# Kernel optimization log

Hardware: AMD Instinct MI355X
Metric: run time of the kernel (lower is better)

## Reference

```python
import jax, jax.numpy as jnp
import numpy as np

D_MODEL = 1024
NUM_HEADS = 16
HEAD_DIM = D_MODEL // NUM_HEADS
SCALE = 1.0 / np.sqrt(HEAD_DIM).astype(np.float32)


def setup_inputs() -> dict:
    key = jax.random.key(0)
    k1, k2, k3, k4 = jax.random.split(key, 4)
    B, L = 1, 4096
    s = 0.02
    x = jax.random.normal(k1, (B, L, D_MODEL), dtype=jnp.float32)
    W_qkv = jax.random.normal(k2, (D_MODEL, 3 * D_MODEL), dtype=jnp.float32) * s
    W_o = jax.random.normal(k3, (D_MODEL, D_MODEL), dtype=jnp.float32) * s
    b_o = jax.random.normal(k4, (D_MODEL,), dtype=jnp.float32) * s
    return {"x": x, "W_qkv": W_qkv, "W_o": W_o, "b_o": b_o}


def reference(x, W_qkv, W_o, b_o):
    B, L, D = x.shape
    H, Hd = NUM_HEADS, HEAD_DIM
    qkv = x @ W_qkv                          # [B, L, 3D]
    qkv = qkv.reshape(B, L, 3, H, Hd)
    q = jnp.transpose(qkv[:, :, 0], (0, 2, 1, 3))  # [B, H, L, Hd]
    k = jnp.transpose(qkv[:, :, 1], (0, 2, 1, 3))
    v = jnp.transpose(qkv[:, :, 2], (0, 2, 1, 3))
    scores = jnp.einsum("bhqd,bhkd->bhqk", q, k) * SCALE  # [B, H, L, L]
    attn = jax.nn.softmax(scores, axis=-1)
    out = jnp.einsum("bhqk,bhkd->bhqd", attn, v)          # [B, H, L, Hd]
    out = jnp.transpose(out, (0, 2, 1, 3)).reshape(B, L, D)
    return out @ W_o + b_o
```

## Files before the change

### kernel.cpp

```cpp
#include <hip/hip_runtime.h>
#include <stdint.h>


#define L_SEQ 4096
#define DM 1024
#define NHEAD 16
#define HDIM 64
#define ATT_SCALE 0.125f
#define LOG2E 1.4426950408889634f
#define CSC (ATT_SCALE * LOG2E)

typedef __attribute__((ext_vector_type(8))) __bf16 bf16x8;
typedef __attribute__((ext_vector_type(4))) __bf16 bf16x4;
typedef __attribute__((ext_vector_type(4))) float f32x4;
typedef __attribute__((ext_vector_type(8))) float f32x8;
typedef __attribute__((ext_vector_type(4))) short short4v;
typedef __attribute__((ext_vector_type(8))) short short8v;

#define GLL16(g, l) __builtin_amdgcn_global_load_lds( \
    (__attribute__((address_space(1))) void*)(g),     \
    (__attribute__((address_space(3))) void*)(l), 16, 0, 0)

#define MFMA32(a, b, c) __builtin_amdgcn_mfma_f32_16x16x32_bf16((a), (b), (c), 0, 0, 0)

__device__ __forceinline__ short f2bf(float f) {
  uint32_t u = __builtin_bit_cast(uint32_t, f);
  u += 0x7fffu + ((u >> 16) & 1u);
  return (short)(u >> 16);
}

__global__ __launch_bounds__(256)
void prep_kernel(const float* __restrict__ x, short* __restrict__ xb,
                 const float* __restrict__ Wq, short* __restrict__ wqt,
                 const float* __restrict__ Wo, short* __restrict__ wot) {
  __shared__ __align__(16) short tbuf[64 * 66];
  const int tid = threadIdx.x;
  const int blk = blockIdx.x;
  if (blk < 4096) {
    int i = blk * 256 + tid;
    float4 v = ((const float4*)x)[i];
    short4 o;
    o.x = f2bf(v.x); o.y = f2bf(v.y); o.z = f2bf(v.z); o.w = f2bf(v.w);
    ((short4*)xb)[i] = o;
    return;
  }
  const float* W; short* Wt; int N, nb, kb;
  const int K = 1024;
  if (blk < 4096 + 768) {
    int b = blk - 4096;
    W = Wq; Wt = wqt; N = 3072; nb = (b % 48) * 64; kb = (b / 48) * 64;
  } else {
    int b = blk - (4096 + 768);
    W = Wo; Wt = wot; N = 1024; nb = (b % 16) * 64; kb = (b / 16) * 64;
  }
#pragma unroll
  for (int i = 0; i < 16; i++) {
    int idx = tid + i * 256;
    int r = idx >> 6, c = idx & 63;
    tbuf[r * 66 + c] = f2bf(W[(size_t)(kb + r) * N + nb + c]);
  }
  __syncthreads();
#pragma unroll
  for (int i = 0; i < 16; i++) {
    int idx = tid + i * 256;
    int r = idx >> 6, c = idx & 63;
    Wt[(size_t)(nb + r) * K + kb + c] = tbuf[c * 66 + r];
  }
}

__global__ __launch_bounds__(256, 2)
void gemm_qkv(const short* __restrict__ A, const short* __restrict__ Bt,
              short* __restrict__ qkv, short* __restrict__ vtout, int K) {
  __shared__ __align__(16) short As[4096];
  __shared__ __align__(16) short Bs[4096];
  const int tid = threadIdx.x;
  const int lane = tid & 63;
  const int wave = tid >> 6;
  const int quad = lane >> 4;
  const int cl = lane & 15;
  const int m0 = blockIdx.x * 128;
  const int n0 = blockIdx.y * 128;
  const int wm = (wave >> 1) * 64;
  const int wn = (wave & 1) * 64;

  f32x4 acc[4][4] = {};

  for (int kb = 0; kb < K; kb += 32) {
    __syncthreads();
#pragma unroll
    for (int i = 0; i < 2; i++) {
      int ci = i * 256 + tid;
      int row = ci & 127, c = ci >> 7;
      GLL16(A + (size_t)(m0 + row) * K + kb + c * 8, As + ci * 8);
      GLL16(Bt + (size_t)(n0 + row) * K + kb + c * 8, Bs + ci * 8);
    }
    __syncthreads();
    bf16x8 af[4], bfr[4];
#pragma unroll
    for (int t = 0; t < 4; t++) {
      af[t]  = *(const bf16x8*)(As + (quad * 128 + wm + t * 16 + cl) * 8);
      bfr[t] = *(const bf16x8*)(Bs + (quad * 128 + wn + t * 16 + cl) * 8);
    }
#pragma unroll
    for (int mt = 0; mt < 4; mt++)
#pragma unroll
      for (int nt = 0; nt < 4; nt++)
        acc[mt][nt] = MFMA32(af[mt], bfr[nt], acc[mt][nt]);
  }

#pragma unroll
  for (int mt = 0; mt < 4; mt++)
#pragma unroll
    for (int nt = 0; nt < 4; nt++) {
      int col = n0 + wn + nt * 16 + cl;
      int which = col >> 10, hd = col & 63;
      int hidx = (col >> 6) & 15;
      int row0 = m0 + wm + mt * 16 + quad * 4;
      if (which == 2) {
        short4v pk;
#pragma unroll
        for (int r = 0; r < 4; r++) pk[r] = f2bf(acc[mt][nt][r]);
        *(short4v*)(vtout + ((size_t)hidx * HDIM + hd) * L_SEQ + row0) = pk;
      } else {
        float sc = (which == 0) ? CSC : 1.0f;
        size_t base = (((size_t)which * NHEAD + hidx) * L_SEQ) * HDIM + hd;
#pragma unroll
        for (int r = 0; r < 4; r++)
          qkv[base + (size_t)(row0 + r) * HDIM] = f2bf(acc[mt][nt][r] * sc);
      }
    }
}

__global__ __launch_bounds__(256, 2)
void gemm_out(const short* __restrict__ A, const short* __restrict__ Bt,
              float* __restrict__ C, const float* __restrict__ bias, int K) {
  __shared__ __align__(16) short As[4096];
  __shared__ __align__(16) short Bs[2048];
  const int tid = threadIdx.x;
  const int lane = tid & 63;
  const int wave = tid >> 6;
  const int quad = lane >> 4;
  const int cl = lane & 15;
  const int m0 = blockIdx.x * 128;
  const int n0 = blockIdx.y * 64;
  const int wm = (wave >> 1) * 64;
  const int wn = (wave & 1) * 32;
  const int N = 1024;

  f32x4 acc[4][2] = {};

  for (int kb = 0; kb < K; kb += 32) {
    __syncthreads();
#pragma unroll
    for (int i = 0; i < 2; i++) {
      int ci = i * 256 + tid;
      GLL16(A + (size_t)(m0 + (ci & 127)) * K + kb + (ci >> 7) * 8, As + ci * 8);
    }
    GLL16(Bt + (size_t)(n0 + (tid & 63)) * K + kb + (tid >> 6) * 8, Bs + tid * 8);
    __syncthreads();
    bf16x8 af[4], bfr[2];
#pragma unroll
    for (int t = 0; t < 4; t++)
      af[t] = *(const bf16x8*)(As + (quad * 128 + wm + t * 16 + cl) * 8);
#pragma unroll
    for (int t = 0; t < 2; t++)
      bfr[t] = *(const bf16x8*)(Bs + (quad * 64 + wn + t * 16 + cl) * 8);
#pragma unroll
    for (int mt = 0; mt < 4; mt++)
#pragma unroll
      for (int nt = 0; nt < 2; nt++)
        acc[mt][nt] = MFMA32(af[mt], bfr[nt], acc[mt][nt]);
  }

#pragma unroll
  for (int mt = 0; mt < 4; mt++)
#pragma unroll
    for (int nt = 0; nt < 2; nt++) {
      int col = n0 + wn + nt * 16 + cl;
      float b = bias[col];
#pragma unroll
      for (int r = 0; r < 4; r++) {
        int row = m0 + wm + mt * 16 + quad * 4 + r;
        C[(size_t)row * N + col] = acc[mt][nt][r] + b;
      }
    }
}

__global__ __launch_bounds__(256, 4)
void attn_kernel(const short* __restrict__ qkv, const short* __restrict__ vt,
                 short* __restrict__ aout) {
  __shared__ __align__(16) short Ks[2][4096];
  __shared__ __align__(16) short Vs[2][4096];
  const int tid = threadIdx.x, lane = tid & 63, wave = tid >> 6;
  const int quad = lane >> 4, cl = lane & 15;
  const int kg = wave >> 1;
  const int qg = wave & 1;
  const int bid = blockIdx.x;
  const int h  = ((bid & 7) << 1) | ((bid >> 3) & 1);
  const int qb = bid >> 4;
  const short* Qg = qkv + (size_t)h * L_SEQ * HDIM;
  const short* Kg = qkv + ((size_t)NHEAD + h) * L_SEQ * HDIM;
  const short* Vg = vt + (size_t)h * HDIM * L_SEQ;
  const int keyoff = ((cl >> 2) << 3) | (cl & 3);

  bf16x8 qf[2][2];
#pragma unroll
  for (int qs = 0; qs < 2; qs++) {
    int qrow = qb * 64 + qg * 32 + qs * 16 + cl;
    qf[qs][0] = *(const bf16x8*)(Qg + (size_t)qrow * HDIM + quad * 8);
    qf[qs][1] = *(const bf16x8*)(Qg + (size_t)qrow * HDIM + 32 + quad * 8);
  }
  const short8v ov = {0x3F80, 0x3F80, 0x3F80, 0x3F80, 0x3F80, 0x3F80, 0x3F80, 0x3F80};
  const bf16x8 ones = __builtin_bit_cast(bf16x8, ov);
  f32x4 o_l[2] = {};
  f32x4 o_acc[4][2] = {};

  int koff[2][2];
#pragma unroll
  for (int b = 0; b < 2; b++) {
    int krow = kg * 32 + keyoff + b * 4;
    int sw = (krow & 3) | (((krow >> 3) & 1) << 2);
#pragma unroll
    for (int ks = 0; ks < 2; ks++)
      koff[b][ks] = (krow * 8 + ((ks * 4 + quad) ^ sw)) * 8;
  }
  int voff[4];
#pragma unroll
  for (int G = 0; G < 4; G++) {
    int vrow = G * 16 + cl;
    int sw = (vrow & 3) | (((vrow >> 3) & 1) << 2);
    voff[G] = (vrow * 8 + ((kg * 4 + quad) ^ sw)) * 8;
  }

  const short* kp[2]; const short* vp[2]; int ldso[2];
#pragma unroll
  for (int i = 0; i < 2; i++) {
    int ci = i * 256 + tid;
    int row = ci >> 3;
    int sw = (row & 3) | (((row >> 3) & 1) << 2);
    int c = (ci & 7) ^ sw;
    kp[i] = Kg + (size_t)row * HDIM + c * 8;
    vp[i] = Vg + (size_t)row * L_SEQ + c * 8;
    ldso[i] = ci * 8;
  }
#define STAGE(t, buf)                                       \
  {                                                         \
    _Pragma("unroll")                                       \
    for (int i = 0; i < 2; i++) {                           \
      GLL16(kp[i] + (t) * 64 * HDIM, &Ks[buf][ldso[i]]);    \
      GLL16(vp[i] + (t) * 64, &Vs[buf][ldso[i]]);           \
    }                                                       \
  }

  STAGE(0, 0);
#pragma unroll 2
  for (int t = 0; t < L_SEQ / 64; t++) {
    const int cur = t & 1;
    __syncthreads();
    if (t + 1 < L_SEQ / 64) STAGE(t + 1, cur ^ 1);
    const short* Kb = Ks[cur];
    const short* Vb = Vs[cur];

    f32x4 s[2][2] = {};
    __builtin_amdgcn_s_setprio(1);
#pragma unroll
    for (int b = 0; b < 2; b++)
#pragma unroll
      for (int ks = 0; ks < 2; ks++) {
        bf16x8 kf = *(const bf16x8*)(Kb + koff[b][ks]);
#pragma unroll
        for (int qs = 0; qs < 2; qs++)
          s[qs][b] = MFMA32(kf, qf[qs][ks], s[qs][b]);
      }
    __builtin_amdgcn_s_setprio(0);

    bf16x8 vfr[4];
#pragma unroll
    for (int G = 0; G < 4; G++)
      vfr[G] = *(const bf16x8*)(Vb + voff[G]);

    bf16x8 pb0;
    {
      f32x8 pv8;
#pragma unroll
      for (int b = 0; b < 2; b++)
#pragma unroll
        for (int r = 0; r < 4; r++)
          pv8[b * 4 + r] = __builtin_amdgcn_exp2f(s[0][b][r]);
      pb0 = __builtin_convertvector(pv8, bf16x8);
    }

    __builtin_amdgcn_s_setprio(1);
    o_l[0] = MFMA32(ones, pb0, o_l[0]);
#pragma unroll
    for (int G = 0; G < 4; G++)
      o_acc[G][0] = MFMA32(vfr[G], pb0, o_acc[G][0]);
    __builtin_amdgcn_s_setprio(0);

    bf16x8 pb1;
    {
      f32x8 pv8;
#pragma unroll
      for (int b = 0; b < 2; b++)
#pragma unroll
        for (int r = 0; r < 4; r++)
          pv8[b * 4 + r] = __builtin_amdgcn_exp2f(s[1][b][r]);
      pb1 = __builtin_convertvector(pv8, bf16x8);
    }

    __builtin_amdgcn_s_setprio(1);
    o_l[1] = MFMA32(ones, pb1, o_l[1]);
#pragma unroll
    for (int G = 0; G < 4; G++)
      o_acc[G][1] = MFMA32(vfr[G], pb1, o_acc[G][1]);
    __builtin_amdgcn_s_setprio(0);
  }
#undef STAGE

  __syncthreads();
  float* ored = (float*)&Ks[0][0];
  float* lred = (float*)&Vs[0][0];
  if (kg == 1) {
#pragma unroll
    for (int G = 0; G < 4; G++)
#pragma unroll
      for (int qs = 0; qs < 2; qs++)
        *(f32x4*)&ored[(((qg * 4 + G) * 2 + qs) * 64 + lane) * 4] = o_acc[G][qs];
#pragma unroll
    for (int qs = 0; qs < 2; qs++)
      lred[(qg * 2 + qs) * 64 + lane] = o_l[qs][0];
  }
  __syncthreads();
  if (kg == 0) {
#pragma unroll
    for (int qs = 0; qs < 2; qs++) {
      float l = o_l[qs][0] + lred[(qg * 2 + qs) * 64 + lane];
      float inv = 1.f / l;
      int token = qb * 64 + qg * 32 + qs * 16 + cl;
#pragma unroll
      for (int G = 0; G < 4; G++) {
        f32x4 part = *(const f32x4*)&ored[(((qg * 4 + G) * 2 + qs) * 64 + lane) * 4];
        f32x4 sc = (o_acc[G][qs] + part) * inv;
        bf16x4 pk = __builtin_convertvector(sc, bf16x4);
        *(short4v*)(aout + (size_t)token * DM + h * HDIM + G * 16 + quad * 4) =
            __builtin_bit_cast(short4v, pk);
      }
    }
  }
}

extern "C" void kernel_launch(void* const* d_in, const int* in_sizes, int n_in,
                              void* d_out, int out_size, void* d_ws, size_t ws_size,
                              hipStream_t stream) {
  const float* x    = (const float*)d_in[0];
  const float* Wqkv = (const float*)d_in[1];
  const float* Wo   = (const float*)d_in[2];
  const float* bo   = (const float*)d_in[3];
  char* ws = (char*)d_ws;
  short* xb    = (short*)(ws);
  short* wqkvt = (short*)(ws + (size_t)8 * 1024 * 1024);
  short* wot   = (short*)(ws + (size_t)14 * 1024 * 1024);
  short* qkv   = (short*)(ws + (size_t)16 * 1024 * 1024);
  short* vt    = (short*)(ws + (size_t)40 * 1024 * 1024);
  short* aout  = xb;
  float* out = (float*)d_out;

  prep_kernel<<<4096 + 768 + 256, 256, 0, stream>>>(x, xb, Wqkv, wqkvt, Wo, wot);
  gemm_qkv<<<dim3(32, 24), 256, 0, stream>>>(xb, wqkvt, qkv, vt, DM);
  attn_kernel<<<dim3(1024), 256, 0, stream>>>(qkv, vt, aout);
  gemm_out<<<dim3(32, 16), 256, 0, stream>>>(aout, wot, out, bo, DM);
}
```

Baseline: 243.6 us.

## Enlarge attention block to 128 queries and 128-key tiles with 8 waves

The attention kernel now runs 512 threads per block covering 128 query rows, and stages 128-key K/V tiles in shared memory, so each staged tile is reused by twice as many queries. Each wave processes two 32-key slabs per tile, and grid size halves to 512 blocks. The intent is to cut global/L2 K/V traffic and the number of barriers per key. In exchange it doubles LDS per block and halves the block count, which may lower occupancy and leave CUs underfilled.

```diff
diff --git a/kernel.cpp b/kernel.cpp
--- a/kernel.cpp
+++ b/kernel.cpp
@@ -186,15 +186,17 @@
     }
 }
 
-__global__ __launch_bounds__(256, 4)
+#define KVB 128
+__global__ __launch_bounds__(512, 4)
 void attn_kernel(const short* __restrict__ qkv, const short* __restrict__ vt,
                  short* __restrict__ aout) {
-  __shared__ __align__(16) short Ks[2][4096];
-  __shared__ __align__(16) short Vs[2][4096];
+  __shared__ __align__(16) short Ks[2][KVB * HDIM];
+  __shared__ __align__(16) short Vs[2][HDIM * KVB];
+  __shared__ float lbuf[512];
   const int tid = threadIdx.x, lane = tid & 63, wave = tid >> 6;
   const int quad = lane >> 4, cl = lane & 15;
-  const int kg = wave >> 1;
-  const int qg = wave & 1;
+  const int kg = wave & 1;
+  const int qg = wave >> 1;
   const int bid = blockIdx.x;
   const int h  = ((bid & 7) << 1) | ((bid >> 3) & 1);
   const int qb = bid >> 4;
@@ -206,7 +208,7 @@
   bf16x8 qf[2][2];
 #pragma unroll
   for (int qs = 0; qs < 2; qs++) {
-    int qrow = qb * 64 + qg * 32 + qs * 16 + cl;
+    int qrow = qb * 128 + qg * 32 + qs * 16 + cl;
     qf[qs][0] = *(const bf16x8*)(Qg + (size_t)qrow * HDIM + quad * 8);
     qf[qs][1] = *(const bf16x8*)(Qg + (size_t)qrow * HDIM + 32 + quad * 8);
   }
@@ -215,111 +217,121 @@
   f32x4 o_l[2] = {};
   f32x4 o_acc[4][2] = {};
 
-  int koff[2][2];
-#pragma unroll
-  for (int b = 0; b < 2; b++) {
-    int krow = kg * 32 + keyoff + b * 4;
-    int sw = (krow & 3) | (((krow >> 3) & 1) << 2);
-#pragma unroll
-    for (int ks = 0; ks < 2; ks++)
-      koff[b][ks] = (krow * 8 + ((ks * 4 + quad) ^ sw)) * 8;
-  }
-  int voff[4];
-#pragma unroll
-  for (int G = 0; G < 4; G++) {
-    int vrow = G * 16 + cl;
-    int sw = (vrow & 3) | (((vrow >> 3) & 1) << 2);
-    voff[G] = (vrow * 8 + ((kg * 4 + quad) ^ sw)) * 8;
-  }
-
-  const short* kp[2]; const short* vp[2]; int ldso[2];
+  int koff[2][2][2];
+  int voff[2][4];
+#pragma unroll
+  for (int kslab = 0; kslab < 2; kslab++) {
+#pragma unroll
+    for (int b = 0; b < 2; b++) {
+      int krow = kg * 64 + kslab * 32 + keyoff + b * 4;
+      int sw = (krow & 3) | (((krow >> 3) & 1) << 2);
+#pragma unroll
+      for (int ks = 0; ks < 2; ks++)
+        koff[kslab][b][ks] = (krow * 8 + ((ks * 4 + quad) ^ sw)) * 8;
+    }
+#pragma unroll
+    for (int G = 0; G < 4; G++) {
+      int vrow = G * 16 + cl;
+      int sw = (vrow & 3) | (((vrow >> 3) & 1) << 2);
+      voff[kslab][G] = (vrow * 16 + ((kg * 8 + kslab * 4 + quad) ^ sw)) * 8;
+    }
+  }
+
+  const short* kp[2]; const short* vp[2]; int ldsoK[2], ldsoV[2];
 #pragma unroll
   for (int i = 0; i < 2; i++) {
-    int ci = i * 256 + tid;
-    int row = ci >> 3;
-    int sw = (row & 3) | (((row >> 3) & 1) << 2);
-    int c = (ci & 7) ^ sw;
-    kp[i] = Kg + (size_t)row * HDIM + c * 8;
-    vp[i] = Vg + (size_t)row * L_SEQ + c * 8;
-    ldso[i] = ci * 8;
-  }
-#define STAGE(t, buf)                                       \
-  {                                                         \
-    _Pragma("unroll")                                       \
-    for (int i = 0; i < 2; i++) {                           \
-      GLL16(kp[i] + (t) * 64 * HDIM, &Ks[buf][ldso[i]]);    \
-      GLL16(vp[i] + (t) * 64, &Vs[buf][ldso[i]]);           \
-    }                                                       \
+    int ciK = i * 512 + tid;
+    int rowK = ciK >> 3;
+    int swK = (rowK & 3) | (((rowK >> 3) & 1) << 2);
+    int cK = (ciK & 7) ^ swK;
+    kp[i] = Kg + (size_t)rowK * HDIM + cK * 8;
+    ldsoK[i] = ciK * 8;
+    int ciV = i * 512 + tid;
+    int rowV = ciV >> 4;
+    int swV = (rowV & 3) | (((rowV >> 3) & 1) << 2);
+    int cV = (ciV & 15) ^ swV;
+    vp[i] = Vg + (size_t)rowV * L_SEQ + cV * 8;
+    ldsoV[i] = ciV * 8;
+  }
+#define STAGE(t, buf)                                        \
+  {                                                          \
+    _Pragma("unroll")                                        \
+    for (int i = 0; i < 2; i++) {                            \
+      GLL16(kp[i] + (t) * KVB * HDIM, &Ks[buf][ldsoK[i]]);   \
+      GLL16(vp[i] + (t) * KVB, &Vs[buf][ldsoV[i]]);          \
+    }                                                        \
   }
 
   STAGE(0, 0);
 #pragma unroll 2
-  for (int t = 0; t < L_SEQ / 64; t++) {
+  for (int t = 0; t < L_SEQ / KVB; t++) {
     const int cur = t & 1;
     __syncthreads();
-    if (t + 1 < L_SEQ / 64) STAGE(t + 1, cur ^ 1);
+    if (t + 1 < L_SEQ / KVB) STAGE(t + 1, cur ^ 1);
     const short* Kb = Ks[cur];
     const short* Vb = Vs[cur];
 
-    f32x4 s[2][2] = {};
-    __builtin_amdgcn_s_setprio(1);
-#pragma unroll
-    for (int b = 0; b < 2; b++)
-#pragma unroll
-      for (int ks = 0; ks < 2; ks++) {
-        bf16x8 kf = *(const bf16x8*)(Kb + koff[b][ks]);
-#pragma unroll
-        for (int qs = 0; qs < 2; qs++)
-          s[qs][b] = MFMA32(kf, qf[qs][ks], s[qs][b]);
-      }
-    __builtin_amdgcn_s_setprio(0);
-
-    bf16x8 vfr[4];
-#pragma unroll
-    for (int G = 0; G < 4; G++)
-      vfr[G] = *(const bf16x8*)(Vb + voff[G]);
-
-    bf16x8 pb0;
-    {
-      f32x8 pv8;
+#pragma unroll
+    for (int kslab = 0; kslab < 2; kslab++) {
+      f32x4 s[2][2] = {};
+      __builtin_amdgcn_s_setprio(1);
 #pragma unroll
       for (int b = 0; b < 2; b++)
 #pragma unroll
-        for (int r = 0; r < 4; r++)
-          pv8[b * 4 + r] = __builtin_amdgcn_exp2f(s[0][b][r]);
-      pb0 = __builtin_convertvector(pv8, bf16x8);
-    }
-
-    __builtin_amdgcn_s_setprio(1);
-    o_l[0] = MFMA32(ones, pb0, o_l[0]);
-#pragma unroll
-    for (int G = 0; G < 4; G++)
-      o_acc[G][0] = MFMA32(vfr[G], pb0, o_acc[G][0]);
-    __builtin_amdgcn_s_setprio(0);
-
-    bf16x8 pb1;
-    {
-      f32x8 pv8;
-#pragma unroll
-      for (int b = 0; b < 2; b++)
-#pragma unroll
-        for (int r = 0; r < 4; r++)
-          pv8[b * 4 + r] = __builtin_amdgcn_exp2f(s[1][b][r]);
-      pb1 = __builtin_convertvector(pv8, bf16x8);
-    }
-
-    __builtin_amdgcn_s_setprio(1);
-    o_l[1] = MFMA32(ones, pb1, o_l[1]);
-#pragma unroll
-    for (int G = 0; G < 4; G++)
-      o_acc[G][1] = MFMA32(vfr[G], pb1, o_acc[G][1]);
-    __builtin_amdgcn_s_setprio(0);
+        for (int ks = 0; ks < 2; ks++) {
+          bf16x8 kf = *(const bf16x8*)(Kb + koff[kslab][b][ks]);
+#pragma unroll
+          for (int qs = 0; qs < 2; qs++)
+            s[qs][b] = MFMA32(kf, qf[qs][ks], s[qs][b]);
+        }
+      __builtin_amdgcn_s_setprio(0);
+
+      bf16x8 vfr[4];
+#pragma unroll
+      for (int G = 0; G < 4; G++)
+        vfr[G] = *(const bf16x8*)(Vb + voff[kslab][G]);
+
+      bf16x8 pb0;
+      {
+        f32x8 pv8;
+#pragma unroll
+        for (int b = 0; b < 2; b++)
+#pragma unroll
+          for (int r = 0; r < 4; r++)
+            pv8[b * 4 + r] = __builtin_amdgcn_exp2f(s[0][b][r]);
+        pb0 = __builtin_convertvector(pv8, bf16x8);
+      }
+
+      __builtin_amdgcn_s_setprio(1);
+      o_l[0] = MFMA32(ones, pb0, o_l[0]);
+#pragma unroll
+      for (int G = 0; G < 4; G++)
+        o_acc[G][0] = MFMA32(vfr[G], pb0, o_acc[G][0]);
+      __builtin_amdgcn_s_setprio(0);
+
+      bf16x8 pb1;
+      {
+        f32x8 pv8;
+#pragma unroll
+        for (int b = 0; b < 2; b++)
+#pragma unroll
+          for (int r = 0; r < 4; r++)
+            pv8[b * 4 + r] = __builtin_amdgcn_exp2f(s[1][b][r]);
+        pb1 = __builtin_convertvector(pv8, bf16x8);
+      }
+
+      __builtin_amdgcn_s_setprio(1);
+      o_l[1] = MFMA32(ones, pb1, o_l[1]);
+#pragma unroll
+      for (int G = 0; G < 4; G++)
+        o_acc[G][1] = MFMA32(vfr[G], pb1, o_acc[G][1]);
+      __builtin_amdgcn_s_setprio(0);
+    }
   }
 #undef STAGE
 
   __syncthreads();
   float* ored = (float*)&Ks[0][0];
-  float* lred = (float*)&Vs[0][0];
   if (kg == 1) {
 #pragma unroll
     for (int G = 0; G < 4; G++)
@@ -328,15 +340,15 @@
         *(f32x4*)&ored[(((qg * 4 + G) * 2 + qs) * 64 + lane) * 4] = o_acc[G][qs];
 #pragma unroll
     for (int qs = 0; qs < 2; qs++)
-      lred[(qg * 2 + qs) * 64 + lane] = o_l[qs][0];
+      lbuf[(qg * 2 + qs) * 64 + lane] = o_l[qs][0];
   }
   __syncthreads();
   if (kg == 0) {
 #pragma unroll
     for (int qs = 0; qs < 2; qs++) {
-      float l = o_l[qs][0] + lred[(qg * 2 + qs) * 64 + lane];
+      float l = o_l[qs][0] + lbuf[(qg * 2 + qs) * 64 + lane];
       float inv = 1.f / l;
-      int token = qb * 64 + qg * 32 + qs * 16 + cl;
+      int token = qb * 128 + qg * 32 + qs * 16 + cl;
 #pragma unroll
       for (int G = 0; G < 4; G++) {
         f32x4 part = *(const f32x4*)&ored[(((qg * 4 + G) * 2 + qs) * 64 + lane) * 4];
@@ -367,6 +379,6 @@
 
   prep_kernel<<<4096 + 768 + 256, 256, 0, stream>>>(x, xb, Wqkv, wqkvt, Wo, wot);
   gemm_qkv<<<dim3(32, 24), 256, 0, stream>>>(xb, wqkvt, qkv, vt, DM);
-  attn_kernel<<<dim3(1024), 256, 0, stream>>>(qkv, vt, aout);
+  attn_kernel<<<dim3(512), 512, 0, stream>>>(qkv, vt, aout);
   gemm_out<<<dim3(32, 16), 256, 0, stream>>>(aout, wot, out, bo, DM);
 }
```

Result: faster. 233.2 us (-4.3%).
